# Performance work log

Hardware: AMD Instinct MI355X
Metric: run time of the kernel (lower is better)

Reference implementation:

```python
import jax, jax.numpy as jnp
import numpy as np

B, S = 32768, 512  # rays, max bright spots (= 2*max_samples)


def setup_inputs() -> dict:
    key = jax.random.key(0)
    k1, k2, k3, k4, k5 = jax.random.split(key, 5)
    V = jax.random.normal(k1, (B, 3), dtype=jnp.float32)
    N = jax.random.normal(k2, (B, 3), dtype=jnp.float32)
    N = N / jnp.linalg.norm(N, axis=-1, keepdims=True)
    spots = jax.random.normal(k3, (S, 3), dtype=jnp.float32)
    spots = spots / jnp.linalg.norm(spots, axis=-1, keepdims=True)
    # prefix masks: num_ele[i] <= num_ray[i] <= S (matches kernel's start_ind-j indexing)
    num_ray = jax.random.randint(k4, (B,), S // 2, S + 1)
    num_ele = jax.random.randint(k5, (B,), 0, S // 2)
    j = jnp.arange(S)
    ray_mask = j[None, :] < num_ray[:, None]
    bright_mask = j[None, :] < num_ele[:, None]
    std = jnp.float32(0.05)  # pix_size
    return {"V": V, "N": N, "spots": spots, "ray_mask": ray_mask,
            "bright_mask": bright_mask, "std": std}


def reference(V, N, spots, ray_mask, bright_mask, std):
    Bn, Sn = bright_mask.shape
    # wp.randf(seed): uniform in [0,1), one per written component -> (B,S,3)
    u = jax.random.uniform(jax.random.key(42), (Bn, Sn, 3), dtype=spots.dtype)
    num_ele = bright_mask.sum(axis=1)            # n per row
    num_ray = ray_mask.sum(axis=1)               # start_ind = num_ray - 1
    j = jnp.arange(Sn)
    active = j[None, :] < num_ele[:, None]       # j in range(n)
    jit = spots[None, :, :] + std * u            # jittered light dirs (B,S,3)
    LdotN = jnp.einsum('bsd,bd->bs', jit, N)
    cond = active & (LdotN > 0.0)                # rejection test
    t = num_ray[:, None] - 1 - j[None, :]        # reversed write index
    t_safe = jnp.where(cond & (t >= 0) & (t < Sn), t, Sn)  # Sn -> dropped
    b_idx = jnp.arange(Bn)[:, None]
    Ls = jnp.zeros((Bn, Sn, 3), spots.dtype).at[b_idx, t_safe].set(jit, mode='drop')
    bmask = jnp.zeros((Bn, Sn), jnp.int32).at[b_idx, t_safe].set(1, mode='drop')
    return Ls, bmask.astype(bool)
```

## Files before the change

### kernel.cpp

```cpp
#include <hip/hip_runtime.h>


#define TF_ROUND(x0, x1, r) { x0 += x1; x1 = ((x1 << (r)) | (x1 >> (32 - (r)))); x1 ^= x0; }

__device__ __forceinline__ unsigned tf2x32_seed42_xor(unsigned x0, unsigned x1) {
  const unsigned k0 = 0u, k1 = 42u;
  const unsigned k2 = 0x1BD11BDAu ^ k0 ^ k1;
  x0 += k0; x1 += k1;
  TF_ROUND(x0,x1,13) TF_ROUND(x0,x1,15) TF_ROUND(x0,x1,26) TF_ROUND(x0,x1,6)
  x0 += k1; x1 += k2 + 1u;
  TF_ROUND(x0,x1,17) TF_ROUND(x0,x1,29) TF_ROUND(x0,x1,16) TF_ROUND(x0,x1,24)
  x0 += k2; x1 += k0 + 2u;
  TF_ROUND(x0,x1,13) TF_ROUND(x0,x1,15) TF_ROUND(x0,x1,26) TF_ROUND(x0,x1,6)
  x0 += k0; x1 += k1 + 3u;
  TF_ROUND(x0,x1,17) TF_ROUND(x0,x1,29) TF_ROUND(x0,x1,16) TF_ROUND(x0,x1,24)
  x0 += k1; x1 += k2 + 4u;
  TF_ROUND(x0,x1,13) TF_ROUND(x0,x1,15) TF_ROUND(x0,x1,26) TF_ROUND(x0,x1,6)
  x0 += k2; x1 += k0 + 5u;
  return x0 ^ x1;
}

typedef float f4v __attribute__((ext_vector_type(4)));

__device__ __forceinline__ int detect_mode(const unsigned char* m) {
  const unsigned char d0 = m[0], d1 = m[1], d4 = m[4];
  return (d0 == 0) ? 3 : ((d1 != 0) ? 0 : ((d4 != 0) ? 1 : 2));
}

__global__ __launch_bounds__(512) void bis_kernel_v(
    const float* __restrict__ Nrm, const float* __restrict__ spots,
    const unsigned char* __restrict__ rmask, const unsigned char* __restrict__ emask,
    const float* __restrict__ stdp, float* __restrict__ Ls, float* __restrict__ bm,
    int B)
{
  const int tid = threadIdx.x;
  const int rib = tid >> 7;
  const int tr  = tid & 127;
  const int b   = blockIdx.x * 4 + rib;
  const int t0  = tr << 2;
  const unsigned base = (unsigned)b * 512u + (unsigned)t0;

  const int mode = detect_mode(rmask);

  int rcnt = 0, ecnt = 0;
  if (b < B) {
    if (mode == 0) {
      const unsigned rv = *(const unsigned*)(rmask + base);
      const unsigned ev = *(const unsigned*)(emask + base);
      rcnt = __popc(rv & 0x01010101u);
      ecnt = __popc(ev & 0x01010101u);
    } else if (mode == 1) {
      const int* rp = (const int*)rmask; const int* ep = (const int*)emask;
      const int4 rv = *(const int4*)(rp + base);
      const int4 ev = *(const int4*)(ep + base);
      rcnt = (rv.x!=0)+(rv.y!=0)+(rv.z!=0)+(rv.w!=0);
      ecnt = (ev.x!=0)+(ev.y!=0)+(ev.z!=0)+(ev.w!=0);
    } else if (mode == 3) {
      const float* rp = (const float*)rmask; const float* ep = (const float*)emask;
      const float4 rv = *(const float4*)(rp + base);
      const float4 ev = *(const float4*)(ep + base);
      rcnt = (rv.x!=0.f)+(rv.y!=0.f)+(rv.z!=0.f)+(rv.w!=0.f);
      ecnt = (ev.x!=0.f)+(ev.y!=0.f)+(ev.z!=0.f)+(ev.w!=0.f);
    } else {
      const long long* rp = (const long long*)rmask; const long long* ep = (const long long*)emask;
      #pragma unroll
      for (int c = 0; c < 4; ++c) { rcnt += rp[base+c] != 0; ecnt += ep[base+c] != 0; }
    }
  }

  unsigned pack = (unsigned)rcnt | ((unsigned)ecnt << 16);
  #pragma unroll
  for (int off = 1; off < 64; off <<= 1) pack += __shfl_xor(pack, off, 64);

  __shared__ unsigned s_pack[8];
  if ((tid & 63) == 0) s_pack[tid >> 6] = pack;
  __syncthreads();
  if (b >= B) return;
  const unsigned rowsum = s_pack[rib * 2] + s_pack[rib * 2 + 1];
  const int num_ray = (int)(rowsum & 0xFFFFu);
  const int num_ele = (int)(rowsum >> 16);

  float o[12];
  #pragma unroll
  for (int i = 0; i < 12; ++i) o[i] = 0.f;
  f4v mk = {0.f, 0.f, 0.f, 0.f};

  const int jhi = num_ray - 1 - t0;
  if (jhi >= 0 && (jhi - 3) < num_ele) {
    const float stdv = stdp[0];
    const float n0 = Nrm[b*3+0], n1 = Nrm[b*3+1], n2 = Nrm[b*3+2];
    #pragma unroll
    for (int c = 0; c < 4; ++c) {
      const int j = jhi - c;
      if (j >= 0 && j < num_ele) {
        const unsigned f = ((unsigned)b * 512u + (unsigned)j) * 3u;
        const float u0 = __uint_as_float((tf2x32_seed42_xor(0u, f + 0u) >> 9) | 0x3F800000u) - 1.0f;
        const float u1 = __uint_as_float((tf2x32_seed42_xor(0u, f + 1u) >> 9) | 0x3F800000u) - 1.0f;
        const float u2 = __uint_as_float((tf2x32_seed42_xor(0u, f + 2u) >> 9) | 0x3F800000u) - 1.0f;
        const float j0 = __fadd_rn(spots[j*3+0], __fmul_rn(stdv, u0));
        const float j1 = __fadd_rn(spots[j*3+1], __fmul_rn(stdv, u1));
        const float j2 = __fadd_rn(spots[j*3+2], __fmul_rn(stdv, u2));
        const float d  = __fadd_rn(__fadd_rn(__fmul_rn(j0,n0), __fmul_rn(j1,n1)),
                                   __fmul_rn(j2,n2));
        if (d > 0.0f) { o[c*3+0]=j0; o[c*3+1]=j1; o[c*3+2]=j2; mk[c]=1.0f; }
      }
    }
  }

  const f4v v0 = {o[0], o[1], o[2],  o[3]};
  const f4v v1 = {o[4], o[5], o[6],  o[7]};
  const f4v v2 = {o[8], o[9], o[10], o[11]};
  f4v* lp = (f4v*)(Ls + (size_t)base * 3u);
  __builtin_nontemporal_store(v0, lp + 0);
  __builtin_nontemporal_store(v1, lp + 1);
  __builtin_nontemporal_store(v2, lp + 2);
  __builtin_nontemporal_store(mk, (f4v*)(bm + base));
}

struct F3 { float x, y, z; };

__global__ __launch_bounds__(512) void bis_kernel_s(
    const float* __restrict__ Nrm, const float* __restrict__ spots,
    const unsigned char* __restrict__ rmask, const unsigned char* __restrict__ emask,
    const float* __restrict__ stdp, float* __restrict__ Ls, float* __restrict__ bm,
    int S)
{
  const long long b = blockIdx.x;
  const int t = threadIdx.x;
  const int mode = detect_mode(rmask);

  const long long e = b * (long long)S + t;
  int rnz, enz;
  if (mode == 0)      { rnz = rmask[e] != 0;                     enz = emask[e] != 0; }
  else if (mode == 1) { rnz = ((const int*)rmask)[e] != 0;       enz = ((const int*)emask)[e] != 0; }
  else if (mode == 2) { rnz = ((const long long*)rmask)[e] != 0; enz = ((const long long*)emask)[e] != 0; }
  else                { rnz = ((const float*)rmask)[e] != 0.0f;  enz = ((const float*)emask)[e] != 0.0f; }

  __shared__ int s_nr[16], s_ne[16];
  const unsigned long long br = __ballot(rnz);
  const unsigned long long be = __ballot(enz);
  const int w = t >> 6;
  if ((t & 63) == 0) { s_nr[w] = __popcll(br); s_ne[w] = __popcll(be); }
  __syncthreads();
  const int nw = blockDim.x >> 6;
  int num_ray = 0, num_ele = 0;
  for (int i = 0; i < nw; ++i) { num_ray += s_nr[i]; num_ele += s_ne[i]; }

  const int j = num_ray - 1 - t;
  float o0 = 0.f, o1 = 0.f, o2 = 0.f, m = 0.f;
  if (j >= 0 && j < num_ele) {
    const float stdv = stdp[0];
    const float n0 = Nrm[b*3+0], n1 = Nrm[b*3+1], n2 = Nrm[b*3+2];
    const unsigned f = (unsigned)((b * (long long)S + j) * 3LL);
    const float u0 = __uint_as_float((tf2x32_seed42_xor(0u, f + 0u) >> 9) | 0x3F800000u) - 1.0f;
    const float u1 = __uint_as_float((tf2x32_seed42_xor(0u, f + 1u) >> 9) | 0x3F800000u) - 1.0f;
    const float u2 = __uint_as_float((tf2x32_seed42_xor(0u, f + 2u) >> 9) | 0x3F800000u) - 1.0f;
    const float j0 = __fadd_rn(spots[j*3+0], __fmul_rn(stdv, u0));
    const float j1 = __fadd_rn(spots[j*3+1], __fmul_rn(stdv, u1));
    const float j2 = __fadd_rn(spots[j*3+2], __fmul_rn(stdv, u2));
    const float d  = __fadd_rn(__fadd_rn(__fmul_rn(j0,n0), __fmul_rn(j1,n1)), __fmul_rn(j2,n2));
    if (d > 0.0f) { o0 = j0; o1 = j1; o2 = j2; m = 1.0f; }
  }

  const long long oidx = b * (long long)S + t;
  F3 v; v.x = o0; v.y = o1; v.z = o2;
  reinterpret_cast<F3*>(Ls)[oidx] = v;
  bm[oidx] = m;
}

extern "C" void kernel_launch(void* const* d_in, const int* in_sizes, int n_in,
                              void* d_out, int out_size, void* d_ws, size_t ws_size,
                              hipStream_t stream) {
  const float* Nrm = (const float*)d_in[1];
  const float* spots = (const float*)d_in[2];
  const unsigned char* rmask = (const unsigned char*)d_in[3];
  const unsigned char* emask = (const unsigned char*)d_in[4];
  const float* stdp = (const float*)d_in[5];

  const int B = in_sizes[0] / 3;
  const int S = in_sizes[2] / 3;

  float* out = (float*)d_out;
  float* Ls = out;
  float* bm = out + (long long)B * S * 3;

  if (S == 512) {
    dim3 grid((unsigned)((B + 3) / 4)), block(512);
    hipLaunchKernelGGL(bis_kernel_v, grid, block, 0, stream,
                       Nrm, spots, rmask, emask, stdp, Ls, bm, B);
  } else {
    dim3 grid((unsigned)B), block((unsigned)S);
    hipLaunchKernelGGL(bis_kernel_s, grid, block, 0, stream,
                       Nrm, spots, rmask, emask, stdp, Ls, bm, S);
  }
}
```

Baseline: 98.85 us.

## Stage jittered spots in shared memory to balance RNG work and coalesce stores

Each of the 128 threads per ray now computes jittered spots for indices j in a strided loop over num_ele and writes them to a 32 KB shared buffer. A second phase gathers the reversed entries from shared memory, so each thread writes consecutive float4 chunks of the Ls row instead of three adjacent vectors per thread. This evens out the threefry work, which used to fall only on threads whose window overlapped the active range, and makes the global stores fully contiguous across lanes. In exchange it adds an extra barrier, 32 KB of LDS per block that may lower occupancy, and drops the nontemporal store hints.

```diff
diff --git a/kernel.cpp b/kernel.cpp
--- a/kernel.cpp
+++ b/kernel.cpp
@@ -27,7 +27,7 @@
   return (d0 == 0) ? 3 : ((d1 != 0) ? 0 : ((d4 != 0) ? 1 : 2));
 }
 
-__global__ __launch_bounds__(512) void bis_kernel_v(
+__global__ __launch_bounds__(512) void bis_kernel_v4(
     const float* __restrict__ Nrm, const float* __restrict__ spots,
     const unsigned char* __restrict__ rmask, const unsigned char* __restrict__ emask,
     const float* __restrict__ stdp, float* __restrict__ Ls, float* __restrict__ bm,
@@ -37,28 +37,29 @@
   const int rib = tid >> 7;
   const int tr  = tid & 127;
   const int b   = blockIdx.x * 4 + rib;
-  const int t0  = tr << 2;
-  const unsigned base = (unsigned)b * 512u + (unsigned)t0;
+  const bool valid = (b < B);
+  const unsigned base = (unsigned)b * 512u + (unsigned)(tr << 2);
+
+  __shared__ float s_jit[4][512][4];
+  __shared__ unsigned s_pack[8];
 
   const int mode = detect_mode(rmask);
 
   int rcnt = 0, ecnt = 0;
-  if (b < B) {
+  if (valid) {
     if (mode == 0) {
       const unsigned rv = *(const unsigned*)(rmask + base);
       const unsigned ev = *(const unsigned*)(emask + base);
       rcnt = __popc(rv & 0x01010101u);
       ecnt = __popc(ev & 0x01010101u);
     } else if (mode == 1) {
-      const int* rp = (const int*)rmask; const int* ep = (const int*)emask;
-      const int4 rv = *(const int4*)(rp + base);
-      const int4 ev = *(const int4*)(ep + base);
+      const int4 rv = *(const int4*)((const int*)rmask + base);
+      const int4 ev = *(const int4*)((const int*)emask + base);
       rcnt = (rv.x!=0)+(rv.y!=0)+(rv.z!=0)+(rv.w!=0);
       ecnt = (ev.x!=0)+(ev.y!=0)+(ev.z!=0)+(ev.w!=0);
     } else if (mode == 3) {
-      const float* rp = (const float*)rmask; const float* ep = (const float*)emask;
-      const float4 rv = *(const float4*)(rp + base);
-      const float4 ev = *(const float4*)(ep + base);
+      const float4 rv = *(const float4*)((const float*)rmask + base);
+      const float4 ev = *(const float4*)((const float*)emask + base);
       rcnt = (rv.x!=0.f)+(rv.y!=0.f)+(rv.z!=0.f)+(rv.w!=0.f);
       ecnt = (ev.x!=0.f)+(ev.y!=0.f)+(ev.z!=0.f)+(ev.w!=0.f);
     } else {
@@ -67,54 +68,66 @@
       for (int c = 0; c < 4; ++c) { rcnt += rp[base+c] != 0; ecnt += ep[base+c] != 0; }
     }
   }
-
   unsigned pack = (unsigned)rcnt | ((unsigned)ecnt << 16);
   #pragma unroll
   for (int off = 1; off < 64; off <<= 1) pack += __shfl_xor(pack, off, 64);
-
-  __shared__ unsigned s_pack[8];
   if ((tid & 63) == 0) s_pack[tid >> 6] = pack;
   __syncthreads();
-  if (b >= B) return;
   const unsigned rowsum = s_pack[rib * 2] + s_pack[rib * 2 + 1];
   const int num_ray = (int)(rowsum & 0xFFFFu);
   const int num_ele = (int)(rowsum >> 16);
 
-  float o[12];
-  #pragma unroll
-  for (int i = 0; i < 12; ++i) o[i] = 0.f;
-  f4v mk = {0.f, 0.f, 0.f, 0.f};
-
-  const int jhi = num_ray - 1 - t0;
-  if (jhi >= 0 && (jhi - 3) < num_ele) {
+  if (valid && num_ele > 0) {
     const float stdv = stdp[0];
     const float n0 = Nrm[b*3+0], n1 = Nrm[b*3+1], n2 = Nrm[b*3+2];
+    for (int j = tr; j < num_ele; j += 128) {
+      const unsigned f = ((unsigned)b * 512u + (unsigned)j) * 3u;
+      const float u0 = __uint_as_float((tf2x32_seed42_xor(0u, f + 0u) >> 9) | 0x3F800000u) - 1.0f;
+      const float u1 = __uint_as_float((tf2x32_seed42_xor(0u, f + 1u) >> 9) | 0x3F800000u) - 1.0f;
+      const float u2 = __uint_as_float((tf2x32_seed42_xor(0u, f + 2u) >> 9) | 0x3F800000u) - 1.0f;
+      const float j0 = __fadd_rn(spots[j*3+0], __fmul_rn(stdv, u0));
+      const float j1 = __fadd_rn(spots[j*3+1], __fmul_rn(stdv, u1));
+      const float j2 = __fadd_rn(spots[j*3+2], __fmul_rn(stdv, u2));
+      const float d  = __fadd_rn(__fadd_rn(__fmul_rn(j0,n0), __fmul_rn(j1,n1)),
+                                 __fmul_rn(j2,n2));
+      const bool acc = (d > 0.0f);
+      f4v e;
+      e.x = acc ? j0 : 0.f; e.y = acc ? j1 : 0.f; e.z = acc ? j2 : 0.f;
+      e.w = acc ? 1.f : 0.f;
+      *(f4v*)(&s_jit[rib][j][0]) = e;
+    }
+  }
+  __syncthreads();
+
+  if (!valid) return;
+
+  const float* jrow = &s_jit[rib][0][0];
+  f4v* lsrow = (f4v*)(Ls + (size_t)b * 1536u);
+  #pragma unroll
+  for (int i = 0; i < 3; ++i) {
+    const int g = i * 128 + tr;
+    const unsigned f = (unsigned)(g << 2);
+    f4v o;
     #pragma unroll
-    for (int c = 0; c < 4; ++c) {
-      const int j = jhi - c;
-      if (j >= 0 && j < num_ele) {
-        const unsigned f = ((unsigned)b * 512u + (unsigned)j) * 3u;
-        const float u0 = __uint_as_float((tf2x32_seed42_xor(0u, f + 0u) >> 9) | 0x3F800000u) - 1.0f;
-        const float u1 = __uint_as_float((tf2x32_seed42_xor(0u, f + 1u) >> 9) | 0x3F800000u) - 1.0f;
-        const float u2 = __uint_as_float((tf2x32_seed42_xor(0u, f + 2u) >> 9) | 0x3F800000u) - 1.0f;
-        const float j0 = __fadd_rn(spots[j*3+0], __fmul_rn(stdv, u0));
-        const float j1 = __fadd_rn(spots[j*3+1], __fmul_rn(stdv, u1));
-        const float j2 = __fadd_rn(spots[j*3+2], __fmul_rn(stdv, u2));
-        const float d  = __fadd_rn(__fadd_rn(__fmul_rn(j0,n0), __fmul_rn(j1,n1)),
-                                   __fmul_rn(j2,n2));
-        if (d > 0.0f) { o[c*3+0]=j0; o[c*3+1]=j1; o[c*3+2]=j2; mk[c]=1.0f; }
-      }
-    }
-  }
-
-  const f4v v0 = {o[0], o[1], o[2],  o[3]};
-  const f4v v1 = {o[4], o[5], o[6],  o[7]};
-  const f4v v2 = {o[8], o[9], o[10], o[11]};
-  f4v* lp = (f4v*)(Ls + (size_t)base * 3u);
-  __builtin_nontemporal_store(v0, lp + 0);
-  __builtin_nontemporal_store(v1, lp + 1);
-  __builtin_nontemporal_store(v2, lp + 2);
-  __builtin_nontemporal_store(mk, (f4v*)(bm + base));
+    for (int k = 0; k < 4; ++k) {
+      const unsigned ff = f + k;
+      const unsigned s  = (ff * 43691u) >> 17;
+      const unsigned comp = ff - 3u * s;
+      const int jj = num_ray - 1 - (int)s;
+      o[k] = (jj >= 0 && jj < num_ele) ? jrow[(unsigned)jj * 4u + comp] : 0.f;
+    }
+    lsrow[g] = o;
+  }
+  {
+    f4v mk;
+    #pragma unroll
+    for (int k = 0; k < 4; ++k) {
+      const int s = (tr << 2) + k;
+      const int jj = num_ray - 1 - s;
+      mk[k] = (jj >= 0 && jj < num_ele) ? jrow[(unsigned)jj * 4u + 3u] : 0.f;
+    }
+    ((f4v*)(bm + (size_t)b * 512u))[tr] = mk;
+  }
 }
 
 struct F3 { float x, y, z; };
@@ -186,7 +199,7 @@
 
   if (S == 512) {
     dim3 grid((unsigned)((B + 3) / 4)), block(512);
-    hipLaunchKernelGGL(bis_kernel_v, grid, block, 0, stream,
+    hipLaunchKernelGGL(bis_kernel_v4, grid, block, 0, stream,
                        Nrm, spots, rmask, emask, stdp, Ls, bm, B);
   } else {
     dim3 grid((unsigned)B), block((unsigned)S);
```

Measured after the change: 91.60 us. 7.3% less time.
